# Kernel optimization log

Hardware: AMD Instinct MI355X
Metric: run time of the kernel (lower is better)

Reference implementation:

```python
import jax, jax.numpy as jnp
import numpy as np

K = 3
PAD = 1
DG = 4
GN_GROUPS = 32
EPS = 1e-5


def deform_conv2d(x, offset, weight):
    # x: [B,C,H,W], offset: [B,DG*2*K*K,H,W] (mmcv layout: per group, per kernel tap, (dy,dx))
    B, C, H, W = x.shape
    KK = K * K
    cg = C // DG
    dt = x.dtype
    off = offset.reshape(B, DG, KK, 2, H, W)
    dy, dx = off[:, :, :, 0], off[:, :, :, 1]  # [B,DG,KK,H,W]
    ky, kx = jnp.meshgrid(jnp.arange(K), jnp.arange(K), indexing='ij')
    ky = ky.reshape(KK).astype(dt)
    kx = kx.reshape(KK).astype(dt)
    hh = jnp.arange(H, dtype=dt)
    ww = jnp.arange(W, dtype=dt)
    # sampling coords: p0 + p_k + offset (stride 1, dilation 1)
    y = hh[None, None, None, :, None] - PAD + ky[None, None, :, None, None] + dy
    xs = ww[None, None, None, None, :] - PAD + kx[None, None, :, None, None] + dx
    y0 = jnp.floor(y)
    x0 = jnp.floor(xs)
    wy1 = y - y0
    wx1 = xs - x0
    xg = x.reshape(B, DG, cg, H * W)

    def corner(yi, xi):
        # zero padding outside the feature map
        valid = (yi >= 0) & (yi < H) & (xi >= 0) & (xi < W)
        yc = jnp.clip(yi, 0, H - 1).astype(jnp.int32)
        xc = jnp.clip(xi, 0, W - 1).astype(jnp.int32)
        idx = (yc * W + xc).reshape(B, DG, KK * H * W)
        v = jax.vmap(jax.vmap(lambda xf, ix: xf[:, ix]))(xg, idx)  # [B,DG,cg,KK*H*W]
        v = v.reshape(B, DG, cg, KK, H, W)
        return v * valid.astype(dt)[:, :, None]

    col = (corner(y0, x0) * ((1 - wy1) * (1 - wx1))[:, :, None]
           + corner(y0, x0 + 1) * ((1 - wy1) * wx1)[:, :, None]
           + corner(y0 + 1, x0) * (wy1 * (1 - wx1))[:, :, None]
           + corner(y0 + 1, x0 + 1) * (wy1 * wx1)[:, :, None])  # [B,DG,cg,KK,H,W]
    col = col.reshape(B, C, KK, H, W)
    O = weight.shape[0]
    return jnp.einsum('ock,bckhw->bohw', weight.reshape(O, C, KK), col)


def group_norm(x, gamma, beta):
    B, C, H, W = x.shape
    xg = x.reshape(B, GN_GROUPS, -1)
    m = xg.mean(-1, keepdims=True)
    v = xg.var(-1, keepdims=True)
    xn = ((xg - m) * jax.lax.rsqrt(v + EPS)).reshape(B, C, H, W)
    return xn * gamma[None, :, None, None] + beta[None, :, None, None]


def setup_inputs() -> dict:
    key = jax.random.key(0)
    k1, k2, k3, k4 = jax.random.split(key, 4)
    B, C, H, W = 4, 256, 64, 64
    x = jax.random.normal(k1, (B, C, H, W), dtype=jnp.float32)
    shape = jax.random.normal(k2, (B, 4, H, W), dtype=jnp.float32)
    w_offset = jax.random.normal(k3, (DG * 2 * K * K, 4), dtype=jnp.float32) * 0.01
    w_deform = jax.random.normal(k4, (C, C, K, K), dtype=jnp.float32) * 0.01
    gamma = jnp.ones((C,), jnp.float32)
    beta = jnp.zeros((C,), jnp.float32)
    return {"x": x, "shape": shape, "w_offset": w_offset, "w_deform": w_deform, "gamma": gamma, "beta": beta}


def reference(x, shape, w_offset, w_deform, gamma, beta):
    # conv_offset: 1x1 conv on detached `shape`
    offset = jnp.einsum('oi,bihw->bohw', w_offset, jax.lax.stop_gradient(shape))
    out = deform_conv2d(x, offset, w_deform)
    return jax.nn.relu(group_norm(out, gamma, beta))
```

## Files before the change

### kernel.cpp

```cpp
#include <hip/hip_runtime.h>
#include <stdint.h>

#define BB   4
#define CCH  256
#define HH   64
#define WWD  64
#define HWSZ 4096
#define DGRP 4
#define CG   64
#define KKN  9
#define KT   2304
#define NND  16384
#define GNG  32
#define EPSV 1e-5f

#define WS_COLT  0
#define WS_WB    75497472
#define WS_G     76677120
#define WS_PART  93454336

typedef __attribute__((ext_vector_type(8))) short short8;
typedef __attribute__((ext_vector_type(4))) float f32x4;

__device__ inline unsigned short f2bf(float f) {
    union { float f; unsigned u; } v; v.f = f;
    unsigned u = v.u;
    return (unsigned short)((u + 0x7FFFu + ((u >> 16) & 1u)) >> 16);
}

__device__ inline float bflo(unsigned u) {
    union { unsigned u; float f; } v; v.u = u << 16; return v.f;
}
__device__ inline float bfhi(unsigned u) {
    union { unsigned u; float f; } v; v.u = u & 0xffff0000u; return v.f;
}

__device__ inline void gl_lds16(const void* g, void* l) {
    __builtin_amdgcn_global_load_lds(
        (const __attribute__((address_space(1))) void*)g,
        (__attribute__((address_space(3))) void*)l,
        16, 0, 0);
}

__global__ __launch_bounds__(256) void col_kernel(const float* __restrict__ x,
                                                  const float* __restrict__ shp,
                                                  const float* __restrict__ woff,
                                                  unsigned short* __restrict__ colT,
                                                  const float* __restrict__ wd,
                                                  unsigned short* __restrict__ Wb) {
    __shared__ __align__(16) unsigned short xt[4 * 12 * 64 * 4];

    int bid = blockIdx.x;
    int tid = threadIdx.x;

    if (bid >= 512) {
        int base = (bid - 512) * 1024 + tid * 4;
        unsigned short t[4];
        #pragma unroll
        for (int u = 0; u < 4; ++u) {
            int idx = base + u;
            int o  = idx / KT;
            int r  = idx % KT;
            int kk = r >> 8;
            int c  = r & 255;
            t[u] = f2bf(wd[o * KT + c * KKN + kk]);
        }
        *(uint2*)&Wb[base] = *(const uint2*)t;
        return;
    }

    int band  = bid & 7;
    int cq    = (bid >> 3) & 3;
    int dg    = (bid >> 5) & 3;
    int b     = bid >> 7;
    int h0    = band * 8;
    int lane  = tid & 63;
    int wv    = tid >> 6;

    const float* xg = x + (size_t)(b * CCH + dg * CG + cq * 16) * HWSZ;
    #pragma unroll 1
    for (int ii = 0; ii < 6; ++ii) {
        float v[8]; int la[8];
        #pragma unroll
        for (int u = 0; u < 8; ++u) {
            int idx = (ii * 8 + u) * 256 + tid;
            int j   = idx / 768;
            int rem = idx - j * 768;
            int r   = rem >> 6;
            int w   = rem & 63;
            int gr  = min(max(h0 - 2 + r, 0), HH - 1);
            v[u]  = xg[(size_t)j * HWSZ + gr * 64 + w];
            la[u] = ((j >> 2) * 12 + r) * 256 + w * 4 + (j & 3);
        }
        #pragma unroll
        for (int u = 0; u < 8; ++u) xt[la[u]] = f2bf(v[u]);
    }
    __syncthreads();

    const char* xtb = (const char*)xt;

    #pragma unroll 1
    for (int hr = 0; hr < 2; ++hr) {
        int h  = h0 + wv * 2 + hr;
        int hw = h * 64 + lane;
        float s0 = shp[(b * 4 + 0) * HWSZ + hw];
        float s1 = shp[(b * 4 + 1) * HWSZ + hw];
        float s2 = shp[(b * 4 + 2) * HWSZ + hw];
        float s3 = shp[(b * 4 + 3) * HWSZ + hw];

        unsigned short* rowp = colT + (size_t)(b * HWSZ + hw) * KT + dg * CG + cq * 16;

        #pragma unroll
        for (int kk = 0; kk < KKN; ++kk) {
            const float* wo = woff + (dg * 18 + kk * 2) * 4;
            float dy = wo[0] * s0 + wo[1] * s1 + wo[2] * s2 + wo[3] * s3;
            float dx = wo[4] * s0 + wo[5] * s1 + wo[6] * s2 + wo[7] * s3;

            int ky = kk / 3, kx = kk % 3;
            float y  = (float)(h - 1 + ky) + dy;
            float xs = (float)(lane - 1 + kx) + dx;
            float y0f = floorf(y), x0f = floorf(xs);
            float wy1 = y - y0f,  wx1 = xs - x0f;
            float wy0 = 1.f - wy1, wx0 = 1.f - wx1;
            int iy0 = (int)y0f, ix0 = (int)x0f;
            int iy1 = iy0 + 1,  ix1 = ix0 + 1;
            bool vy0 = (iy0 >= 0) && (iy0 < HH);
            bool vy1 = (iy1 >= 0) && (iy1 < HH);
            bool vx0 = (ix0 >= 0) && (ix0 < WWD);
            bool vx1 = (ix1 >= 0) && (ix1 < WWD);
            float w00 = (vy0 && vx0) ? wy0 * wx0 : 0.f;
            float w01 = (vy0 && vx1) ? wy0 * wx1 : 0.f;
            float w10 = (vy1 && vx0) ? wy1 * wx0 : 0.f;
            float w11 = (vy1 && vx1) ? wy1 * wx1 : 0.f;
            int cy0 = min(max(iy0, 0), HH - 1);
            int cy1 = min(max(iy1, 0), HH - 1);
            int cx0 = min(max(ix0, 0), WWD - 1);
            int cx1 = min(max(ix1, 0), WWD - 1);
            int ty0 = min(max(cy0 - (h0 - 2), 0), 11);
            int ty1 = min(max(cy1 - (h0 - 2), 0), 11);
            int a00 = (ty0 * 64 + cx0) * 8;
            int a01 = (ty0 * 64 + cx1) * 8;
            int a10 = (ty1 * 64 + cx0) * 8;
            int a11 = (ty1 * 64 + cx1) * 8;

            unsigned short tmp[16];
            #pragma unroll
            for (int c4g = 0; c4g < 4; ++c4g) {
                int base = c4g * 6144;
                const uint2 q00 = *(const uint2*)(xtb + base + a00);
                const uint2 q01 = *(const uint2*)(xtb + base + a01);
                const uint2 q10 = *(const uint2*)(xtb + base + a10);
                const uint2 q11 = *(const uint2*)(xtb + base + a11);
                float r0 = w00 * bflo(q00.x) + w01 * bflo(q01.x) + w10 * bflo(q10.x) + w11 * bflo(q11.x);
                float r1 = w00 * bfhi(q00.x) + w01 * bfhi(q01.x) + w10 * bfhi(q10.x) + w11 * bfhi(q11.x);
                float r2 = w00 * bflo(q00.y) + w01 * bflo(q01.y) + w10 * bflo(q10.y) + w11 * bflo(q11.y);
                float r3 = w00 * bfhi(q00.y) + w01 * bfhi(q01.y) + w10 * bfhi(q10.y) + w11 * bfhi(q11.y);
                tmp[c4g * 4 + 0] = f2bf(r0);
                tmp[c4g * 4 + 1] = f2bf(r1);
                tmp[c4g * 4 + 2] = f2bf(r2);
                tmp[c4g * 4 + 3] = f2bf(r3);
            }
            uint4* dst = (uint4*)(rowp + kk * 256);
            const uint4* src = (const uint4*)tmp;
            dst[0] = src[0];
            dst[1] = src[1];
        }
    }
}

__global__ __launch_bounds__(256) void gemm_kernel(const unsigned short* __restrict__ Wb,
                                                   const unsigned short* __restrict__ colT,
                                                   unsigned short* __restrict__ G,
                                                   float* __restrict__ partials) {
    __shared__ __align__(16) short As[64 * 64];
    __shared__ __align__(16) short Bs[128 * 64];
    __shared__ float sred[16];

    int tid  = threadIdx.x;
    int lane = tid & 63;
    int wv   = tid >> 6;
    int wm   = wv >> 1;
    int wn   = wv & 1;

    int idx  = blockIdx.x;
    int xcd  = idx & 7;
    int j2   = idx >> 3;
    int n0   = (xcd * 16 + (j2 >> 2)) * 128;
    int m0   = (j2 & 3) * 64;

    if (tid < 16) sred[tid] = 0.f;

    int r_a = tid >> 3;
    int s_a = tid & 7;
    int k_a = (s_a ^ (r_a & 7)) * 8;

    f32x4 acc[2][4] = {};

    int quad = lane >> 4;
    int lrow = lane & 15;
    int sw   = lrow & 7;

    for (int kt = 0; kt < KT; kt += 64) {
        #pragma unroll
        for (int u = 0; u < 2; ++u) {
            int rr = u * 32 + r_a;
            gl_lds16(Wb + (size_t)(m0 + rr) * KT + kt + k_a,
                     (short*)As + (u * 256 + tid) * 8);
        }
        #pragma unroll
        for (int u = 0; u < 4; ++u) {
            int rr = u * 32 + r_a;
            gl_lds16(colT + (size_t)(n0 + rr) * KT + kt + k_a,
                     (short*)Bs + (u * 256 + tid) * 8);
        }
        __syncthreads();

        #pragma unroll
        for (int kb = 0; kb < 2; ++kb) {
            int slot = (kb * 4 + quad) ^ sw;
            short8 a[2], b[4];
            #pragma unroll
            for (int i = 0; i < 2; ++i)
                a[i] = *(const short8*)&As[(wm * 32 + i * 16 + lrow) * 64 + slot * 8];
            #pragma unroll
            for (int j = 0; j < 4; ++j)
                b[j] = *(const short8*)&Bs[(wn * 64 + j * 16 + lrow) * 64 + slot * 8];
            #pragma unroll
            for (int i = 0; i < 2; ++i)
                #pragma unroll
                for (int j = 0; j < 4; ++j)
                    acc[i][j] = __builtin_amdgcn_mfma_f32_16x16x32_bf16(a[i], b[j], acc[i][j], 0, 0, 0);
        }
        __syncthreads();
    }

    #pragma unroll
    for (int i = 0; i < 2; ++i) {
        int m = m0 + wm * 32 + i * 16 + quad * 4;
        #pragma unroll
        for (int j = 0; j < 4; ++j) {
            int n = n0 + wn * 64 + j * 16 + lrow;
            #pragma unroll
            for (int r = 0; r < 4; ++r)
                G[(size_t)(m + r) * NND + n] = f2bf(acc[i][j][r]);
        }
    }

    #pragma unroll
    for (int i = 0; i < 2; ++i) {
        float s1 = 0.f, s2 = 0.f;
        #pragma unroll
        for (int j = 0; j < 4; ++j)
            #pragma unroll
            for (int r = 0; r < 4; ++r) {
                float v = acc[i][j][r];
                s1 += v;
                s2 += v * v;
            }
        #pragma unroll
        for (int off = 1; off < 16; off <<= 1) {
            s1 += __shfl_xor(s1, off);
            s2 += __shfl_xor(s2, off);
        }
        if (lrow == 0) {
            int gg = (wm * 32 + i * 16 + quad * 4) >> 3;
            atomicAdd(&sred[gg * 2],     s1);
            atomicAdd(&sred[gg * 2 + 1], s2);
        }
    }
    __syncthreads();
    if (tid < 8) {
        int b  = n0 >> 12;
        int g0 = m0 >> 3;
        atomicAdd(&partials[(b * 32 + g0 + tid) * 2],     sred[tid * 2]);
        atomicAdd(&partials[(b * 32 + g0 + tid) * 2 + 1], sred[tid * 2 + 1]);
    }
}

__global__ __launch_bounds__(256) void gn_apply_kernel(const unsigned short* __restrict__ G,
                                                       const float* __restrict__ partials,
                                                       const float* __restrict__ gamma,
                                                       const float* __restrict__ beta,
                                                       float* __restrict__ out) {
    int idx = blockIdx.x * 256 + threadIdx.x;
    int hw4 = idx & 1023;
    int o   = (idx >> 10) & 255;
    int b   = idx >> 18;
    int g   = o >> 3;
    const float invN = 1.f / 32768.f;
    float p1 = partials[(b * 32 + g) * 2];
    float p2 = partials[(b * 32 + g) * 2 + 1];
    float mean = p1 * invN;
    float var  = p2 * invN - mean * mean;
    float rstd = rsqrtf(var + EPSV);
    float ga = gamma[o], be = beta[o];
    const uint2 q = *(const uint2*)&G[(size_t)o * NND + b * HWSZ + hw4 * 4];
    float4 r;
    r.x = fmaxf(0.f, (bflo(q.x) - mean) * rstd * ga + be);
    r.y = fmaxf(0.f, (bfhi(q.x) - mean) * rstd * ga + be);
    r.z = fmaxf(0.f, (bflo(q.y) - mean) * rstd * ga + be);
    r.w = fmaxf(0.f, (bfhi(q.y) - mean) * rstd * ga + be);
    *(float4*)&out[(size_t)(b * CCH + o) * HWSZ + hw4 * 4] = r;
}

extern "C" void kernel_launch(void* const* d_in, const int* in_sizes, int n_in,
                              void* d_out, int out_size, void* d_ws, size_t ws_size,
                              hipStream_t stream) {
    const float* x     = (const float*)d_in[0];
    const float* shp   = (const float*)d_in[1];
    const float* woff  = (const float*)d_in[2];
    const float* wdef  = (const float*)d_in[3];
    const float* gamma = (const float*)d_in[4];
    const float* beta  = (const float*)d_in[5];
    float* out = (float*)d_out;

    char* ws = (char*)d_ws;
    unsigned short* colT = (unsigned short*)(ws + WS_COLT);
    unsigned short* Wb   = (unsigned short*)(ws + WS_WB);
    unsigned short* G    = (unsigned short*)(ws + WS_G);
    float* partials      = (float*)(ws + WS_PART);

    hipMemsetAsync(partials, 0, 128 * 2 * sizeof(float), stream);
    col_kernel<<<1088, 256, 0, stream>>>(x, shp, woff, colT, wdef, Wb);
    gemm_kernel<<<512, 256, 0, stream>>>(Wb, colT, G, partials);
    gn_apply_kernel<<<4096, 256, 0, stream>>>(G, partials, gamma, beta, out);
}
```

Baseline: 140.2 us.

## Fuse GroupNorm apply into GEMM via cooperative grid sync

The GEMM becomes a cooperative kernel. After accumulating the group statistics it synchronises the whole grid, then applies GroupNorm and ReLU directly from the accumulator registers. This removes the bf16 intermediate G buffer write and read and the separate gn_apply launch. The memset of the partials buffer is also folded into col_kernel. In exchange it needs all 512 blocks to be co-resident, it pays for a grid-wide barrier, and the output stores are less coalesced (16 consecutive floats per row segment).

```diff
diff --git a/kernel.cpp b/kernel.cpp
--- a/kernel.cpp
+++ b/kernel.cpp
@@ -1,5 +1,8 @@
 #include <hip/hip_runtime.h>
+#include <hip/hip_cooperative_groups.h>
 #include <stdint.h>
+
+namespace cg = cooperative_groups;
 
 #define BB   4
 #define CCH  256
@@ -16,8 +19,7 @@
 
 #define WS_COLT  0
 #define WS_WB    75497472
-#define WS_G     76677120
-#define WS_PART  93454336
+#define WS_PART  76677120
 
 typedef __attribute__((ext_vector_type(8))) short short8;
 typedef __attribute__((ext_vector_type(4))) float f32x4;
@@ -47,13 +49,15 @@
                                                   const float* __restrict__ woff,
                                                   unsigned short* __restrict__ colT,
                                                   const float* __restrict__ wd,
-                                                  unsigned short* __restrict__ Wb) {
+                                                  unsigned short* __restrict__ Wb,
+                                                  float* __restrict__ partials) {
     __shared__ __align__(16) unsigned short xt[4 * 12 * 64 * 4];
 
     int bid = blockIdx.x;
     int tid = threadIdx.x;
 
     if (bid >= 512) {
+        if (bid == 512) partials[tid] = 0.f;
         int base = (bid - 512) * 1024 + tid * 4;
         unsigned short t[4];
         #pragma unroll
@@ -170,8 +174,10 @@
 
 __global__ __launch_bounds__(256) void gemm_kernel(const unsigned short* __restrict__ Wb,
                                                    const unsigned short* __restrict__ colT,
-                                                   unsigned short* __restrict__ G,
-                                                   float* __restrict__ partials) {
+                                                   float* __restrict__ partials,
+                                                   const float* __restrict__ gamma,
+                                                   const float* __restrict__ beta,
+                                                   float* __restrict__ out) {
     __shared__ __align__(16) short As[64 * 64];
     __shared__ __align__(16) short Bs[128 * 64];
     __shared__ float sred[16];
@@ -236,18 +242,6 @@
 
     #pragma unroll
     for (int i = 0; i < 2; ++i) {
-        int m = m0 + wm * 32 + i * 16 + quad * 4;
-        #pragma unroll
-        for (int j = 0; j < 4; ++j) {
-            int n = n0 + wn * 64 + j * 16 + lrow;
-            #pragma unroll
-            for (int r = 0; r < 4; ++r)
-                G[(size_t)(m + r) * NND + n] = f2bf(acc[i][j][r]);
-        }
-    }
-
-    #pragma unroll
-    for (int i = 0; i < 2; ++i) {
         float s1 = 0.f, s2 = 0.f;
         #pragma unroll
         for (int j = 0; j < 4; ++j)
@@ -269,38 +263,40 @@
         }
     }
     __syncthreads();
+    int b  = n0 >> 12;
     if (tid < 8) {
-        int b  = n0 >> 12;
         int g0 = m0 >> 3;
         atomicAdd(&partials[(b * 32 + g0 + tid) * 2],     sred[tid * 2]);
         atomicAdd(&partials[(b * 32 + g0 + tid) * 2 + 1], sred[tid * 2 + 1]);
     }
-}
-
-__global__ __launch_bounds__(256) void gn_apply_kernel(const unsigned short* __restrict__ G,
-                                                       const float* __restrict__ partials,
-                                                       const float* __restrict__ gamma,
-                                                       const float* __restrict__ beta,
-                                                       float* __restrict__ out) {
-    int idx = blockIdx.x * 256 + threadIdx.x;
-    int hw4 = idx & 1023;
-    int o   = (idx >> 10) & 255;
-    int b   = idx >> 18;
-    int g   = o >> 3;
+
+    cg::this_grid().sync();
+
     const float invN = 1.f / 32768.f;
-    float p1 = partials[(b * 32 + g) * 2];
-    float p2 = partials[(b * 32 + g) * 2 + 1];
-    float mean = p1 * invN;
-    float var  = p2 * invN - mean * mean;
-    float rstd = rsqrtf(var + EPSV);
-    float ga = gamma[o], be = beta[o];
-    const uint2 q = *(const uint2*)&G[(size_t)o * NND + b * HWSZ + hw4 * 4];
-    float4 r;
-    r.x = fmaxf(0.f, (bflo(q.x) - mean) * rstd * ga + be);
-    r.y = fmaxf(0.f, (bfhi(q.x) - mean) * rstd * ga + be);
-    r.z = fmaxf(0.f, (bflo(q.y) - mean) * rstd * ga + be);
-    r.w = fmaxf(0.f, (bfhi(q.y) - mean) * rstd * ga + be);
-    *(float4*)&out[(size_t)(b * CCH + o) * HWSZ + hw4 * 4] = r;
+    int hwb = (n0 & 4095) + wn * 64;
+    #pragma unroll
+    for (int i = 0; i < 2; ++i) {
+        int m = m0 + wm * 32 + i * 16 + quad * 4;
+        int g = m >> 3;
+        volatile const float* pp = partials + (b * 32 + g) * 2;
+        float p1 = pp[0];
+        float p2 = pp[1];
+        float mean = p1 * invN;
+        float var  = p2 * invN - mean * mean;
+        float rstd = rsqrtf(var + EPSV);
+        #pragma unroll
+        for (int r = 0; r < 4; ++r) {
+            int o = m + r;
+            float ga = gamma[o] * rstd;
+            float be = beta[o] - mean * ga;
+            float* orow = out + ((size_t)(b * CCH + o) << 12);
+            #pragma unroll
+            for (int j = 0; j < 4; ++j) {
+                int hw = hwb + j * 16 + lrow;
+                orow[hw] = fmaxf(0.f, acc[i][j][r] * ga + be);
+            }
+        }
+    }
 }
 
 extern "C" void kernel_launch(void* const* d_in, const int* in_sizes, int n_in,
@@ -317,11 +313,12 @@
     char* ws = (char*)d_ws;
     unsigned short* colT = (unsigned short*)(ws + WS_COLT);
     unsigned short* Wb   = (unsigned short*)(ws + WS_WB);
-    unsigned short* G    = (unsigned short*)(ws + WS_G);
     float* partials      = (float*)(ws + WS_PART);
 
-    hipMemsetAsync(partials, 0, 128 * 2 * sizeof(float), stream);
-    col_kernel<<<1088, 256, 0, stream>>>(x, shp, woff, colT, wdef, Wb);
-    gemm_kernel<<<512, 256, 0, stream>>>(Wb, colT, G, partials);
-    gn_apply_kernel<<<4096, 256, 0, stream>>>(G, partials, gamma, beta, out);
-}
+    col_kernel<<<1088, 256, 0, stream>>>(x, shp, woff, colT, wdef, Wb, partials);
+
+    void* args[] = {(void*)&Wb, (void*)&colT, (void*)&partials,
+                    (void*)&gamma, (void*)&beta, (void*)&out};
+    hipLaunchCooperativeKernel((void*)gemm_kernel, dim3(512), dim3(256),
+                               args, 0, stream);
+}
```

New measurement: 200.1 us. +42.7%, slower.
